# Optimization experiments

Measured on AMD Instinct MI355X. Metric: run time of the kernel, lower is better.

Reference implementation:

```python
import jax, jax.numpy as jnp
import numpy as np

N_NODES = 100000


def gcn_conv(x, W, b, src, dst, n_nodes):
    # PyG GCNConv: h = x @ W; out = D^-1/2 (A + I) D^-1/2 h + b
    h = x @ W  # [N, F_out]
    e_ones = jnp.ones(src.shape[0], dtype=x.dtype)
    deg = jax.ops.segment_sum(e_ones, dst, num_segments=n_nodes) + 1.0  # self-loop
    dinv = jax.lax.rsqrt(deg)  # [N]
    norm = dinv[src] * dinv[dst]  # [E]
    msg = h[src] * norm[:, None]  # [E, F_out] (memory-bound gather)
    agg = jax.ops.segment_sum(msg, dst, num_segments=n_nodes)
    agg = agg + h * (dinv * dinv)[:, None]  # self-loop contribution
    return agg + b


def setup_inputs() -> dict:
    key = jax.random.key(0)
    ks = jax.random.split(key, 9)
    in_dim, h1, h2, out_dim = 512, 256, 128, 64
    n_edges = 1_600_000
    x = jax.random.normal(ks[0], (N_NODES, in_dim), dtype=jnp.float32)
    edge_index = jax.random.randint(ks[1], (2, n_edges), 0, N_NODES, dtype=jnp.int32)
    def glorot(k, fi, fo):
        s = float(np.sqrt(6.0 / (fi + fo)))
        return jax.random.uniform(k, (fi, fo), jnp.float32, -s, s)
    return {
        "x": x,
        "edge_index": edge_index,
        "W1": glorot(ks[2], in_dim, h1), "b1": jnp.zeros((h1,), jnp.float32),
        "W2": glorot(ks[3], h1, h2), "b2": jnp.zeros((h2,), jnp.float32),
        "W3": glorot(ks[4], h2, out_dim), "b3": jnp.zeros((out_dim,), jnp.float32),
    }


def reference(x, edge_index, W1, b1, W2, b2, W3, b3):
    src, dst = edge_index[0], edge_index[1]
    h = gcn_conv(x, W1, b1, src, dst, N_NODES)
    h = jax.nn.relu(h)  # dropout omitted (eval mode)
    h = gcn_conv(h, W2, b2, src, dst, N_NODES)
    h = jax.nn.relu(h)
    h = gcn_conv(h, W3, b3, src, dst, N_NODES)
    return jax.nn.log_softmax(h, axis=1)
```

## Files before the change

### kernel.cpp

```cpp
#include <hip/hip_runtime.h>
#include <hip/hip_bf16.h>

#define NN 100000
#define MP 100096

typedef unsigned short u16;
typedef __attribute__((ext_vector_type(8))) short bf16x8;
typedef __attribute__((ext_vector_type(4))) float f32x4;

static inline size_t align_up(size_t x, size_t a) { return (x + a - 1) & ~(a - 1); }

__device__ inline u16 f2b(float f) {
    unsigned u = __float_as_uint(f);
    return (u16)((u + 0x7FFF + ((u >> 16) & 1)) >> 16);
}
__device__ inline float b2f(u16 u) { return __uint_as_float(((unsigned)u) << 16); }


__global__ __launch_bounds__(256) void deg_count_kernel(const int* __restrict__ dst,
                                                        int* __restrict__ deg, int E) {
    int t = blockIdx.x * 256 + threadIdx.x;
    if (t < E) atomicAdd(&deg[dst[t]], 1);
}

__global__ __launch_bounds__(256) void dinv_kernel(const int* __restrict__ deg,
                                                   float* __restrict__ dinv, int n) {
    int t = blockIdx.x * 256 + threadIdx.x;
    if (t < n) dinv[t] = rsqrtf((float)deg[t] + 1.0f);
}

__global__ __launch_bounds__(256) void scan_phase1(const int* __restrict__ deg,
                                                   int* __restrict__ partials, int n4) {
    __shared__ int red[256];
    const int t = threadIdx.x;
    const int g = blockIdx.x * 256 + t;
    int4 v = make_int4(0, 0, 0, 0);
    if (g < n4) v = ((const int4*)deg)[g];
    red[t] = v.x + v.y + v.z + v.w;
    __syncthreads();
    #pragma unroll
    for (int d = 128; d; d >>= 1) {
        if (t < d) red[t] += red[t + d];
        __syncthreads();
    }
    if (t == 0) partials[blockIdx.x] = red[0];
}

__global__ __launch_bounds__(128) void scan_phase2(int* __restrict__ partials,
                                                   int* __restrict__ rowptr, int nb, int n) {
    __shared__ int ps[128];
    const int t = threadIdx.x;
    int v = (t < nb) ? partials[t] : 0;
    ps[t] = v;
    __syncthreads();
    #pragma unroll
    for (int d = 1; d < 128; d <<= 1) {
        int u = (t >= d) ? ps[t - d] : 0;
        __syncthreads();
        ps[t] += u;
        __syncthreads();
    }
    if (t < nb) partials[t] = ps[t] - v;
    if (t == nb - 1) rowptr[n] = ps[t];
}

__global__ __launch_bounds__(256) void scan_phase3(const int* __restrict__ deg,
                                                   const int* __restrict__ partials,
                                                   int* __restrict__ rowptr, int n4) {
    __shared__ int ts[256];
    const int t = threadIdx.x;
    const int g = blockIdx.x * 256 + t;
    int4 v = make_int4(0, 0, 0, 0);
    if (g < n4) v = ((const int4*)deg)[g];
    const int s0 = v.x, s1 = s0 + v.y, s2 = s1 + v.z, s3 = s2 + v.w;
    ts[t] = s3;
    __syncthreads();
    #pragma unroll
    for (int d = 1; d < 256; d <<= 1) {
        int u = (t >= d) ? ts[t - d] : 0;
        __syncthreads();
        ts[t] += u;
        __syncthreads();
    }
    if (g < n4) {
        const int base = partials[blockIdx.x] + ts[t] - s3;
        int4 r;
        r.x = base; r.y = base + s0; r.z = base + s1; r.w = base + s2;
        ((int4*)rowptr)[g] = r;
    }
}

__global__ __launch_bounds__(256) void reorder_kernel(const int* __restrict__ src,
        const int* __restrict__ dst, const int* __restrict__ rowptr,
        int* __restrict__ cursor, const float* __restrict__ dinv,
        int2* __restrict__ erec, int E) {
    int e = blockIdx.x * 256 + threadIdx.x;
    if (e >= E) return;
    int s = src[e], d = dst[e];
    int pos = rowptr[d] + atomicAdd(&cursor[d], 1);
    erec[pos] = make_int2(s, __float_as_int(dinv[s] * dinv[d]));
}


__global__ __launch_bounds__(256) void cvt_kernel(const float* __restrict__ in,
                                                  u16* __restrict__ out, int n8) {
    int t = blockIdx.x * 256 + threadIdx.x;
    if (t >= n8) return;
    const float4* p = (const float4*)in + 2 * (size_t)t;
    float4 a = p[0], b = p[1];
    bf16x8 v;
    v[0] = (short)f2b(a.x); v[1] = (short)f2b(a.y); v[2] = (short)f2b(a.z); v[3] = (short)f2b(a.w);
    v[4] = (short)f2b(b.x); v[5] = (short)f2b(b.y); v[6] = (short)f2b(b.z); v[7] = (short)f2b(b.w);
    *(bf16x8*)(out + 8 * (size_t)t) = v;
}

__global__ __launch_bounds__(256) void transpose_kernel(const float* __restrict__ W,
                                                        u16* __restrict__ WT, int K, int N) {
    int t = blockIdx.x * 256 + threadIdx.x;
    if (t >= K * N) return;
    int n = t / K, k = t - n * K;
    WT[t] = f2b(W[(size_t)k * N + n]);
}

__global__ __launch_bounds__(256) void gemm_mfma(const u16* __restrict__ A,
        const u16* __restrict__ BT, u16* __restrict__ C, int K, int ldc) {
    __shared__ char lds[32768];
    char* Al = lds;
    char* Bl = lds + 16384;
    const int tid = threadIdx.x;
    const int l = tid & 63;
    const int w = tid >> 6;
    const int wm = w >> 1, wn = w & 1;
    const long bm = (long)blockIdx.x * 128;
    const long bn = (long)blockIdx.y * 128;

    f32x4 acc[4][4];
    #pragma unroll
    for (int mi = 0; mi < 4; ++mi)
        #pragma unroll
        for (int ni = 0; ni < 4; ++ni)
            acc[mi][ni] = (f32x4){0.f, 0.f, 0.f, 0.f};

    const int srow = tid >> 3;
    const int schunk = (tid & 7) << 4;

    for (int k0 = 0; k0 < K; k0 += 64) {
        __syncthreads();
        #pragma unroll
        for (int i = 0; i < 4; ++i) {
            const int row = i * 32 + srow;
            const int lb = schunk ^ ((row & 7) << 4);
            const u16* ga = A + (bm + row) * K + k0 + (lb >> 1);
            const u16* gb = BT + (bn + row) * K + k0 + (lb >> 1);
            char* la = Al + i * 4096 + tid * 16;
            char* lbp = Bl + i * 4096 + tid * 16;
            __builtin_amdgcn_global_load_lds((const __attribute__((address_space(1))) void*)ga,
                                             (__attribute__((address_space(3))) void*)la, 16, 0, 0);
            __builtin_amdgcn_global_load_lds((const __attribute__((address_space(1))) void*)gb,
                                             (__attribute__((address_space(3))) void*)lbp, 16, 0, 0);
        }
        __syncthreads();
        #pragma unroll
        for (int kk = 0; kk < 2; ++kk) {
            const int kbyte = kk * 64 + ((l >> 4) << 4);
            const int swz = (l & 7) << 4;
            bf16x8 af[4], bfr[4];
            #pragma unroll
            for (int mi = 0; mi < 4; ++mi) {
                const int row = wm * 64 + mi * 16 + (l & 15);
                af[mi] = *(const bf16x8*)(Al + row * 128 + (kbyte ^ swz));
            }
            #pragma unroll
            for (int ni = 0; ni < 4; ++ni) {
                const int row = wn * 64 + ni * 16 + (l & 15);
                bfr[ni] = *(const bf16x8*)(Bl + row * 128 + (kbyte ^ swz));
            }
            #pragma unroll
            for (int mi = 0; mi < 4; ++mi)
                #pragma unroll
                for (int ni = 0; ni < 4; ++ni)
                    acc[mi][ni] = __builtin_amdgcn_mfma_f32_16x16x32_bf16(
                        af[mi], bfr[ni], acc[mi][ni], 0, 0, 0);
        }
    }

    const long r0 = bm + wm * 64 + ((l >> 4) << 2);
    const long c0 = bn + wn * 64 + (l & 15);
    #pragma unroll
    for (int mi = 0; mi < 4; ++mi)
        #pragma unroll
        for (int r = 0; r < 4; ++r) {
            const long row = r0 + mi * 16 + r;
            #pragma unroll
            for (int ni = 0; ni < 4; ++ni)
                C[row * ldc + c0 + ni * 16] = f2b(acc[mi][ni][r]);
        }
}


template<int VEC, bool RELU>
__global__ __launch_bounds__(256) void agg_kernel(const u16* __restrict__ h,
        const int* __restrict__ rowptr, const int2* __restrict__ erec,
        const float* __restrict__ dinv, const float* __restrict__ bias,
        u16* __restrict__ out, int N) {
    const int node = blockIdx.x * 4 + (threadIdx.x >> 6);
    if (node >= N) return;
    const int lane = threadIdx.x & 63;
    const int F = 64 * VEC;
    const float di = dinv[node];
    const float d2 = di * di;
    float acc[VEC];
    {
        const u16* hp = h + (size_t)node * F + lane * VEC;
        if constexpr (VEC == 4) {
            ushort4 v = *(const ushort4*)hp;
            float4 b = *(const float4*)(bias + lane * 4);
            acc[0] = b2f(v.x) * d2 + b.x; acc[1] = b2f(v.y) * d2 + b.y;
            acc[2] = b2f(v.z) * d2 + b.z; acc[3] = b2f(v.w) * d2 + b.w;
        } else {
            ushort2 v = *(const ushort2*)hp;
            float2 b = *(const float2*)(bias + lane * 2);
            acc[0] = b2f(v.x) * d2 + b.x; acc[1] = b2f(v.y) * d2 + b.y;
        }
    }
    const int e0 = rowptr[node], e1 = rowptr[node + 1];
    int e = e0;
    for (; e + 4 <= e1; e += 4) {
        int2 r0 = erec[e], r1 = erec[e + 1], r2 = erec[e + 2], r3 = erec[e + 3];
        const u16* p0 = h + (size_t)r0.x * F + lane * VEC;
        const u16* p1 = h + (size_t)r1.x * F + lane * VEC;
        const u16* p2 = h + (size_t)r2.x * F + lane * VEC;
        const u16* p3 = h + (size_t)r3.x * F + lane * VEC;
        const float w0 = __int_as_float(r0.y), w1 = __int_as_float(r1.y);
        const float w2 = __int_as_float(r2.y), w3 = __int_as_float(r3.y);
        if constexpr (VEC == 4) {
            ushort4 v0 = *(const ushort4*)p0;
            ushort4 v1 = *(const ushort4*)p1;
            ushort4 v2 = *(const ushort4*)p2;
            ushort4 v3 = *(const ushort4*)p3;
            acc[0] += b2f(v0.x) * w0; acc[1] += b2f(v0.y) * w0; acc[2] += b2f(v0.z) * w0; acc[3] += b2f(v0.w) * w0;
            acc[0] += b2f(v1.x) * w1; acc[1] += b2f(v1.y) * w1; acc[2] += b2f(v1.z) * w1; acc[3] += b2f(v1.w) * w1;
            acc[0] += b2f(v2.x) * w2; acc[1] += b2f(v2.y) * w2; acc[2] += b2f(v2.z) * w2; acc[3] += b2f(v2.w) * w2;
            acc[0] += b2f(v3.x) * w3; acc[1] += b2f(v3.y) * w3; acc[2] += b2f(v3.z) * w3; acc[3] += b2f(v3.w) * w3;
        } else {
            ushort2 v0 = *(const ushort2*)p0;
            ushort2 v1 = *(const ushort2*)p1;
            ushort2 v2 = *(const ushort2*)p2;
            ushort2 v3 = *(const ushort2*)p3;
            acc[0] += b2f(v0.x) * w0; acc[1] += b2f(v0.y) * w0;
            acc[0] += b2f(v1.x) * w1; acc[1] += b2f(v1.y) * w1;
            acc[0] += b2f(v2.x) * w2; acc[1] += b2f(v2.y) * w2;
            acc[0] += b2f(v3.x) * w3; acc[1] += b2f(v3.y) * w3;
        }
    }
    for (; e < e1; ++e) {
        int2 r = erec[e];
        const float wgt = __int_as_float(r.y);
        const u16* sp = h + (size_t)r.x * F + lane * VEC;
        if constexpr (VEC == 4) {
            ushort4 v = *(const ushort4*)sp;
            acc[0] += b2f(v.x) * wgt; acc[1] += b2f(v.y) * wgt;
            acc[2] += b2f(v.z) * wgt; acc[3] += b2f(v.w) * wgt;
        } else {
            ushort2 v = *(const ushort2*)sp;
            acc[0] += b2f(v.x) * wgt; acc[1] += b2f(v.y) * wgt;
        }
    }
    u16* op = out + (size_t)node * F + lane * VEC;
    if constexpr (VEC == 4) {
        ushort4 r;
        r.x = f2b(RELU ? fmaxf(acc[0], 0.f) : acc[0]);
        r.y = f2b(RELU ? fmaxf(acc[1], 0.f) : acc[1]);
        r.z = f2b(RELU ? fmaxf(acc[2], 0.f) : acc[2]);
        r.w = f2b(RELU ? fmaxf(acc[3], 0.f) : acc[3]);
        *(ushort4*)op = r;
    } else {
        ushort2 r;
        r.x = f2b(RELU ? fmaxf(acc[0], 0.f) : acc[0]);
        r.y = f2b(RELU ? fmaxf(acc[1], 0.f) : acc[1]);
        *(ushort2*)op = r;
    }
}

__global__ __launch_bounds__(256) void agg_lsm_kernel(const u16* __restrict__ h,
        const int* __restrict__ rowptr, const int2* __restrict__ erec,
        const float* __restrict__ dinv, const float* __restrict__ bias,
        float* __restrict__ out, int N) {
    const int node = blockIdx.x * 4 + (threadIdx.x >> 6);
    if (node >= N) return;
    const int lane = threadIdx.x & 63;
    const float di = dinv[node];
    float acc = b2f(h[(size_t)node * 128 + lane]) * di * di + bias[lane];
    const int e0 = rowptr[node], e1 = rowptr[node + 1];
    int e = e0;
    for (; e + 4 <= e1; e += 4) {
        int2 r0 = erec[e], r1 = erec[e + 1], r2 = erec[e + 2], r3 = erec[e + 3];
        float v0 = b2f(h[(size_t)r0.x * 128 + lane]);
        float v1 = b2f(h[(size_t)r1.x * 128 + lane]);
        float v2 = b2f(h[(size_t)r2.x * 128 + lane]);
        float v3 = b2f(h[(size_t)r3.x * 128 + lane]);
        acc += v0 * __int_as_float(r0.y);
        acc += v1 * __int_as_float(r1.y);
        acc += v2 * __int_as_float(r2.y);
        acc += v3 * __int_as_float(r3.y);
    }
    for (; e < e1; ++e) {
        int2 r = erec[e];
        acc += b2f(h[(size_t)r.x * 128 + lane]) * __int_as_float(r.y);
    }
    float m = acc;
    #pragma unroll
    for (int o = 32; o; o >>= 1) m = fmaxf(m, __shfl_xor(m, o, 64));
    float ex = __expf(acc - m);
    float s = ex;
    #pragma unroll
    for (int o = 32; o; o >>= 1) s += __shfl_xor(s, o, 64);
    out[(size_t)node * 64 + lane] = acc - m - __logf(s);
}


extern "C" void kernel_launch(void* const* d_in, const int* in_sizes, int n_in,
                              void* d_out, int out_size, void* d_ws, size_t ws_size,
                              hipStream_t stream) {
    const float* x  = (const float*)d_in[0];
    const int*   ei = (const int*)d_in[1];
    const float* W1 = (const float*)d_in[2];
    const float* b1 = (const float*)d_in[3];
    const float* W2 = (const float*)d_in[4];
    const float* b2 = (const float*)d_in[5];
    const float* W3 = (const float*)d_in[6];
    const float* b3 = (const float*)d_in[7];
    const int E = in_sizes[1] / 2;
    const int* src = ei;
    const int* dst = ei + E;
    const int N = NN;
    const int N4 = N / 4;
    const int NB = (N4 + 255) / 256;

    char* ws = (char*)d_ws;
    int*   deg      = (int*)ws;    ws += align_up((size_t)N * 4, 256);
    int*   cursor   = (int*)ws;    ws += align_up((size_t)N * 4, 256);
    float* dinv     = (float*)ws;  ws += align_up((size_t)N * 4, 256);
    int*   rowptr   = (int*)ws;    ws += align_up((size_t)(N + 1) * 4, 256);
    int*   partials = (int*)ws;    ws += align_up((size_t)128 * 4, 256);
    int2*  erec     = (int2*)ws;   ws += align_up((size_t)E * 8, 256);
    u16*   wt1      = (u16*)ws;    ws += align_up((size_t)256 * 512 * 2, 256);
    u16*   wt2      = (u16*)ws;    ws += align_up((size_t)128 * 256 * 2, 256);
    u16*   wt3      = (u16*)ws;    ws += align_up((size_t)128 * 128 * 2, 256);
    u16*   xb       = (u16*)ws;    ws += (size_t)MP * 512 * 2;
    u16*   bufH     = (u16*)ws;    ws += (size_t)MP * 256 * 2;
    u16*   bufAct   = (u16*)ws;    ws += (size_t)MP * 256 * 2;
    u16*   h2b  = xb;
    u16*   h3b  = bufH;
    float* out  = (float*)d_out;

    hipMemsetAsync(deg, 0, (size_t)N * 4, stream);
    hipMemsetAsync(cursor, 0, (size_t)N * 4, stream);

    deg_count_kernel<<<(E + 255) / 256, 256, 0, stream>>>(dst, deg, E);
    dinv_kernel<<<(N + 255) / 256, 256, 0, stream>>>(deg, dinv, N);
    scan_phase1<<<NB, 256, 0, stream>>>(deg, partials, N4);
    scan_phase2<<<1, 128, 0, stream>>>(partials, rowptr, NB, N);
    scan_phase3<<<NB, 256, 0, stream>>>(deg, partials, rowptr, N4);
    reorder_kernel<<<(E + 255) / 256, 256, 0, stream>>>(src, dst, rowptr, cursor, dinv, erec, E);

    cvt_kernel<<<(N * 512 / 8 + 255) / 256, 256, 0, stream>>>(x, xb, N * 512 / 8);
    transpose_kernel<<<(512 * 256 + 255) / 256, 256, 0, stream>>>(W1, wt1, 512, 256);
    transpose_kernel<<<(256 * 128 + 255) / 256, 256, 0, stream>>>(W2, wt2, 256, 128);
    transpose_kernel<<<(128 * 64 + 255) / 256, 256, 0, stream>>>(W3, wt3, 128, 64);

    const int GB = MP / 128;
    const int AB = (N + 3) / 4;

    gemm_mfma<<<dim3(GB, 2), 256, 0, stream>>>(xb, wt1, bufH, 512, 256);
    agg_kernel<4, true><<<AB, 256, 0, stream>>>(bufH, rowptr, erec, dinv, b1, bufAct, N);

    gemm_mfma<<<dim3(GB, 1), 256, 0, stream>>>(bufAct, wt2, h2b, 256, 128);
    agg_kernel<2, true><<<AB, 256, 0, stream>>>(h2b, rowptr, erec, dinv, b2, bufAct, N);

    gemm_mfma<<<dim3(GB, 1), 256, 0, stream>>>(bufAct, wt3, h3b, 128, 128);
    agg_lsm_kernel<<<AB, 256, 0, stream>>>(h3b, rowptr, erec, dinv, b3, out, N);
}
```

Before: 813.6 us.

## Fuse fp32-to-bf16 input conversion into first GEMM and deepen gather unroll

Removes the standalone cvt_kernel. The first GEMM now reads fp32 x directly, converts it to bf16 in registers and writes it into swizzled LDS. This avoids writing and re-reading a 100 MB bf16 copy of x, at the cost of synchronous register loads in place of async global-to-LDS loads for A. The aggregation kernels also unroll the edge gather to 8 to keep more loads in flight, and the two memsets are merged into one.

```diff
diff --git a/kernel.cpp b/kernel.cpp
--- a/kernel.cpp
+++ b/kernel.cpp
@@ -102,18 +102,6 @@
 }
 
 
-__global__ __launch_bounds__(256) void cvt_kernel(const float* __restrict__ in,
-                                                  u16* __restrict__ out, int n8) {
-    int t = blockIdx.x * 256 + threadIdx.x;
-    if (t >= n8) return;
-    const float4* p = (const float4*)in + 2 * (size_t)t;
-    float4 a = p[0], b = p[1];
-    bf16x8 v;
-    v[0] = (short)f2b(a.x); v[1] = (short)f2b(a.y); v[2] = (short)f2b(a.z); v[3] = (short)f2b(a.w);
-    v[4] = (short)f2b(b.x); v[5] = (short)f2b(b.y); v[6] = (short)f2b(b.z); v[7] = (short)f2b(b.w);
-    *(bf16x8*)(out + 8 * (size_t)t) = v;
-}
-
 __global__ __launch_bounds__(256) void transpose_kernel(const float* __restrict__ W,
                                                         u16* __restrict__ WT, int K, int N) {
     int t = blockIdx.x * 256 + threadIdx.x;
@@ -158,6 +146,96 @@
                                              (__attribute__((address_space(3))) void*)la, 16, 0, 0);
             __builtin_amdgcn_global_load_lds((const __attribute__((address_space(1))) void*)gb,
                                              (__attribute__((address_space(3))) void*)lbp, 16, 0, 0);
+        }
+        __syncthreads();
+        #pragma unroll
+        for (int kk = 0; kk < 2; ++kk) {
+            const int kbyte = kk * 64 + ((l >> 4) << 4);
+            const int swz = (l & 7) << 4;
+            bf16x8 af[4], bfr[4];
+            #pragma unroll
+            for (int mi = 0; mi < 4; ++mi) {
+                const int row = wm * 64 + mi * 16 + (l & 15);
+                af[mi] = *(const bf16x8*)(Al + row * 128 + (kbyte ^ swz));
+            }
+            #pragma unroll
+            for (int ni = 0; ni < 4; ++ni) {
+                const int row = wn * 64 + ni * 16 + (l & 15);
+                bfr[ni] = *(const bf16x8*)(Bl + row * 128 + (kbyte ^ swz));
+            }
+            #pragma unroll
+            for (int mi = 0; mi < 4; ++mi)
+                #pragma unroll
+                for (int ni = 0; ni < 4; ++ni)
+                    acc[mi][ni] = __builtin_amdgcn_mfma_f32_16x16x32_bf16(
+                        af[mi], bfr[ni], acc[mi][ni], 0, 0, 0);
+        }
+    }
+
+    const long r0 = bm + wm * 64 + ((l >> 4) << 2);
+    const long c0 = bn + wn * 64 + (l & 15);
+    #pragma unroll
+    for (int mi = 0; mi < 4; ++mi)
+        #pragma unroll
+        for (int r = 0; r < 4; ++r) {
+            const long row = r0 + mi * 16 + r;
+            #pragma unroll
+            for (int ni = 0; ni < 4; ++ni)
+                C[row * ldc + c0 + ni * 16] = f2b(acc[mi][ni][r]);
+        }
+}
+
+__global__ __launch_bounds__(256) void gemm_mfma_f32a(const float* __restrict__ A32,
+        const u16* __restrict__ BT, u16* __restrict__ C, int K, int ldc) {
+    __shared__ char lds[32768];
+    char* Al = lds;
+    char* Bl = lds + 16384;
+    const int tid = threadIdx.x;
+    const int l = tid & 63;
+    const int w = tid >> 6;
+    const int wm = w >> 1, wn = w & 1;
+    const long bm = (long)blockIdx.x * 128;
+    const long bn = (long)blockIdx.y * 128;
+
+    f32x4 acc[4][4];
+    #pragma unroll
+    for (int mi = 0; mi < 4; ++mi)
+        #pragma unroll
+        for (int ni = 0; ni < 4; ++ni)
+            acc[mi][ni] = (f32x4){0.f, 0.f, 0.f, 0.f};
+
+    const int srow = tid >> 3;
+    const int schunk = (tid & 7) << 4;
+
+    for (int k0 = 0; k0 < K; k0 += 64) {
+        __syncthreads();
+        #pragma unroll
+        for (int i = 0; i < 4; ++i) {
+            const int row = i * 32 + srow;
+            const int lb = schunk ^ ((row & 7) << 4);
+            const u16* gb = BT + (bn + row) * K + k0 + (lb >> 1);
+            char* lbp = Bl + i * 4096 + tid * 16;
+            __builtin_amdgcn_global_load_lds((const __attribute__((address_space(1))) void*)gb,
+                                             (__attribute__((address_space(3))) void*)lbp, 16, 0, 0);
+        }
+        float4 a0[4], a1[4];
+        #pragma unroll
+        for (int i = 0; i < 4; ++i) {
+            const int row = i * 32 + srow;
+            const long ar = (bm + row < NN) ? (bm + row) : (NN - 1);
+            const float* ga = A32 + ar * K + k0 + (schunk >> 1);
+            a0[i] = *(const float4*)ga;
+            a1[i] = *(const float4*)(ga + 4);
+        }
+        #pragma unroll
+        for (int i = 0; i < 4; ++i) {
+            const int row = i * 32 + srow;
+            bf16x8 v;
+            v[0] = (short)f2b(a0[i].x); v[1] = (short)f2b(a0[i].y);
+            v[2] = (short)f2b(a0[i].z); v[3] = (short)f2b(a0[i].w);
+            v[4] = (short)f2b(a1[i].x); v[5] = (short)f2b(a1[i].y);
+            v[6] = (short)f2b(a1[i].z); v[7] = (short)f2b(a1[i].w);
+            *(bf16x8*)(Al + row * 128 + (schunk ^ ((row & 7) << 4))) = v;
         }
         __syncthreads();
         #pragma unroll
@@ -225,32 +303,58 @@
     }
     const int e0 = rowptr[node], e1 = rowptr[node + 1];
     int e = e0;
+    for (; e + 8 <= e1; e += 8) {
+        int2 r[8];
+        #pragma unroll
+        for (int j = 0; j < 8; ++j) r[j] = erec[e + j];
+        if constexpr (VEC == 4) {
+            ushort4 v[8];
+            #pragma unroll
+            for (int j = 0; j < 8; ++j)
+                v[j] = *(const ushort4*)(h + (size_t)r[j].x * F + lane * 4);
+            #pragma unroll
+            for (int j = 0; j < 8; ++j) {
+                const float wj = __int_as_float(r[j].y);
+                acc[0] += b2f(v[j].x) * wj; acc[1] += b2f(v[j].y) * wj;
+                acc[2] += b2f(v[j].z) * wj; acc[3] += b2f(v[j].w) * wj;
+            }
+        } else {
+            ushort2 v[8];
+            #pragma unroll
+            for (int j = 0; j < 8; ++j)
+                v[j] = *(const ushort2*)(h + (size_t)r[j].x * F + lane * 2);
+            #pragma unroll
+            for (int j = 0; j < 8; ++j) {
+                const float wj = __int_as_float(r[j].y);
+                acc[0] += b2f(v[j].x) * wj; acc[1] += b2f(v[j].y) * wj;
+            }
+        }
+    }
     for (; e + 4 <= e1; e += 4) {
-        int2 r0 = erec[e], r1 = erec[e + 1], r2 = erec[e + 2], r3 = erec[e + 3];
-        const u16* p0 = h + (size_t)r0.x * F + lane * VEC;
-        const u16* p1 = h + (size_t)r1.x * F + lane * VEC;
-        const u16* p2 = h + (size_t)r2.x * F + lane * VEC;
-        const u16* p3 = h + (size_t)r3.x * F + lane * VEC;
-        const float w0 = __int_as_float(r0.y), w1 = __int_as_float(r1.y);
-        const float w2 = __int_as_float(r2.y), w3 = __int_as_float(r3.y);
+        int2 r[4];
+        #pragma unroll
+        for (int j = 0; j < 4; ++j) r[j] = erec[e + j];
         if constexpr (VEC == 4) {
-            ushort4 v0 = *(const ushort4*)p0;
-            ushort4 v1 = *(const ushort4*)p1;
-            ushort4 v2 = *(const ushort4*)p2;
-            ushort4 v3 = *(const ushort4*)p3;
-            acc[0] += b2f(v0.x) * w0; acc[1] += b2f(v0.y) * w0; acc[2] += b2f(v0.z) * w0; acc[3] += b2f(v0.w) * w0;
-            acc[0] += b2f(v1.x) * w1; acc[1] += b2f(v1.y) * w1; acc[2] += b2f(v1.z) * w1; acc[3] += b2f(v1.w) * w1;
-            acc[0] += b2f(v2.x) * w2; acc[1] += b2f(v2.y) * w2; acc[2] += b2f(v2.z) * w2; acc[3] += b2f(v2.w) * w2;
-            acc[0] += b2f(v3.x) * w3; acc[1] += b2f(v3.y) * w3; acc[2] += b2f(v3.z) * w3; acc[3] += b2f(v3.w) * w3;
+            ushort4 v[4];
+            #pragma unroll
+            for (int j = 0; j < 4; ++j)
+                v[j] = *(const ushort4*)(h + (size_t)r[j].x * F + lane * 4);
+            #pragma unroll
+            for (int j = 0; j < 4; ++j) {
+                const float wj = __int_as_float(r[j].y);
+                acc[0] += b2f(v[j].x) * wj; acc[1] += b2f(v[j].y) * wj;
+                acc[2] += b2f(v[j].z) * wj; acc[3] += b2f(v[j].w) * wj;
+            }
         } else {
-            ushort2 v0 = *(const ushort2*)p0;
-            ushort2 v1 = *(const ushort2*)p1;
-            ushort2 v2 = *(const ushort2*)p2;
-            ushort2 v3 = *(const ushort2*)p3;
-            acc[0] += b2f(v0.x) * w0; acc[1] += b2f(v0.y) * w0;
-            acc[0] += b2f(v1.x) * w1; acc[1] += b2f(v1.y) * w1;
-            acc[0] += b2f(v2.x) * w2; acc[1] += b2f(v2.y) * w2;
-            acc[0] += b2f(v3.x) * w3; acc[1] += b2f(v3.y) * w3;
+            ushort2 v[4];
+            #pragma unroll
+            for (int j = 0; j < 4; ++j)
+                v[j] = *(const ushort2*)(h + (size_t)r[j].x * F + lane * 2);
+            #pragma unroll
+            for (int j = 0; j < 4; ++j) {
+                const float wj = __int_as_float(r[j].y);
+                acc[0] += b2f(v[j].x) * wj; acc[1] += b2f(v[j].y) * wj;
+            }
         }
     }
     for (; e < e1; ++e) {
@@ -293,16 +397,25 @@
     float acc = b2f(h[(size_t)node * 128 + lane]) * di * di + bias[lane];
     const int e0 = rowptr[node], e1 = rowptr[node + 1];
     int e = e0;
+    for (; e + 8 <= e1; e += 8) {
+        int2 r[8];
+        #pragma unroll
+        for (int j = 0; j < 8; ++j) r[j] = erec[e + j];
+        float v[8];
+        #pragma unroll
+        for (int j = 0; j < 8; ++j) v[j] = b2f(h[(size_t)r[j].x * 128 + lane]);
+        #pragma unroll
+        for (int j = 0; j < 8; ++j) acc += v[j] * __int_as_float(r[j].y);
+    }
     for (; e + 4 <= e1; e += 4) {
-        int2 r0 = erec[e], r1 = erec[e + 1], r2 = erec[e + 2], r3 = erec[e + 3];
-        float v0 = b2f(h[(size_t)r0.x * 128 + lane]);
-        float v1 = b2f(h[(size_t)r1.x * 128 + lane]);
-        float v2 = b2f(h[(size_t)r2.x * 128 + lane]);
-        float v3 = b2f(h[(size_t)r3.x * 128 + lane]);
-        acc += v0 * __int_as_float(r0.y);
-        acc += v1 * __int_as_float(r1.y);
-        acc += v2 * __int_as_float(r2.y);
-        acc += v3 * __int_as_float(r3.y);
+        int2 r[4];
+        #pragma unroll
+        for (int j = 0; j < 4; ++j) r[j] = erec[e + j];
+        float v[4];
+        #pragma unroll
+        for (int j = 0; j < 4; ++j) v[j] = b2f(h[(size_t)r[j].x * 128 + lane]);
+        #pragma unroll
+        for (int j = 0; j < 4; ++j) acc += v[j] * __int_as_float(r[j].y);
     }
     for (; e < e1; ++e) {
         int2 r = erec[e];
@@ -347,15 +460,13 @@
     u16*   wt1      = (u16*)ws;    ws += align_up((size_t)256 * 512 * 2, 256);
     u16*   wt2      = (u16*)ws;    ws += align_up((size_t)128 * 256 * 2, 256);
     u16*   wt3      = (u16*)ws;    ws += align_up((size_t)128 * 128 * 2, 256);
-    u16*   xb       = (u16*)ws;    ws += (size_t)MP * 512 * 2;
     u16*   bufH     = (u16*)ws;    ws += (size_t)MP * 256 * 2;
     u16*   bufAct   = (u16*)ws;    ws += (size_t)MP * 256 * 2;
-    u16*   h2b  = xb;
+    u16*   h2b      = (u16*)ws;    ws += (size_t)MP * 128 * 2;
     u16*   h3b  = bufH;
     float* out  = (float*)d_out;
 
-    hipMemsetAsync(deg, 0, (size_t)N * 4, stream);
-    hipMemsetAsync(cursor, 0, (size_t)N * 4, stream);
+    hipMemsetAsync(deg, 0, 2 * align_up((size_t)N * 4, 256), stream);
 
     deg_count_kernel<<<(E + 255) / 256, 256, 0, stream>>>(dst, deg, E);
     dinv_kernel<<<(N + 255) / 256, 256, 0, stream>>>(deg, dinv, N);
@@ -364,7 +475,6 @@
     scan_phase3<<<NB, 256, 0, stream>>>(deg, partials, rowptr, N4);
     reorder_kernel<<<(E + 255) / 256, 256, 0, stream>>>(src, dst, rowptr, cursor, dinv, erec, E);
 
-    cvt_kernel<<<(N * 512 / 8 + 255) / 256, 256, 0, stream>>>(x, xb, N * 512 / 8);
     transpose_kernel<<<(512 * 256 + 255) / 256, 256, 0, stream>>>(W1, wt1, 512, 256);
     transpose_kernel<<<(256 * 128 + 255) / 256, 256, 0, stream>>>(W2, wt2, 256, 128);
     transpose_kernel<<<(128 * 64 + 255) / 256, 256, 0, stream>>>(W3, wt3, 128, 64);
@@ -372,7 +482,7 @@
     const int GB = MP / 128;
     const int AB = (N + 3) / 4;
 
-    gemm_mfma<<<dim3(GB, 2), 256, 0, stream>>>(xb, wt1, bufH, 512, 256);
+    gemm_mfma_f32a<<<dim3(GB, 2), 256, 0, stream>>>(x, wt1, bufH, 512, 256);
     agg_kernel<4, true><<<AB, 256, 0, stream>>>(bufH, rowptr, erec, dinv, b1, bufAct, N);
 
     gemm_mfma<<<dim3(GB, 1), 256, 0, stream>>>(bufAct, wt2, h2b, 256, 128);
```

Result: faster. 773.6 us (-4.9%).
